# Kernel optimization log

Measured on AMD Instinct MI355X. Metric: run time of the kernel, lower is better.

The kernel has to match this reference:

```python
import jax, jax.numpy as jnp
import numpy as np
from jax import lax

DATA, WIDTH, BATCH, T = 64, 256, 512, 16
MAX_SUBSTEPS = 8
RTOL, ATOL, SAFETY, FMIN, FMAX = 1e-3, 1e-6, 0.9, 0.2, 10.0

# Tsit5 Butcher tableau (Tsitouras 2011), autonomous field so c-nodes unused.
A21 = 0.161
A31, A32 = -0.008480655492356989, 0.335480655492357
A41, A42, A43 = 2.8971530571054935, -6.359448489975075, 4.3622954328695815
A51, A52, A53, A54 = 5.325864828439257, -11.748883564062828, 7.4955393428898365, -0.09249506636175525
A61, A62, A63, A64, A65 = 5.86145544294642, -12.92096931784711, 8.159367898576159, -0.071584973281401, -0.028269050394068383
B1, B2, B3, B4, B5, B6 = 0.09646076681806523, 0.01, 0.4798896504144996, 1.379008574103742, -3.290069515436081, 2.324710524099774
E1, E2, E3, E4, E5, E6, E7 = -0.001780011052226, -0.000816434459657, 0.007880878010262, -0.144711007173263, 0.582357165452555, -0.458082105929187, 0.015151515151515152


def setup_inputs() -> dict:
    key = jax.random.key(0)
    ks = jax.random.split(key, 4)
    ts = jnp.linspace(0.0, 1.0, T, dtype=jnp.float32)
    y0 = jax.random.normal(ks[0], (BATCH, DATA), dtype=jnp.float32)
    s_in = 1.0 / np.sqrt(DATA)
    s_w = 1.0 / np.sqrt(WIDTH)
    W0 = jax.random.normal(ks[1], (WIDTH, DATA), dtype=jnp.float32) * s_in
    b0 = jnp.zeros((WIDTH,), dtype=jnp.float32)
    W1 = jax.random.normal(ks[2], (WIDTH, WIDTH), dtype=jnp.float32) * s_w
    b1 = jnp.zeros((WIDTH,), dtype=jnp.float32)
    W2 = jax.random.normal(ks[3], (DATA, WIDTH), dtype=jnp.float32) * s_w
    b2 = jnp.zeros((DATA,), dtype=jnp.float32)
    return {"ts": ts, "y0": y0, "W0": W0, "b0": b0, "W1": W1, "b1": b1, "W2": W2, "b2": b2}


def _mlp(y, W0, b0, W1, b1, W2, b2):
    h = jax.nn.softplus(W0 @ y + b0)
    h = jax.nn.softplus(W1 @ h + b1)
    return W2 @ h + b2


def _tsit5_step(f, y, dt):
    k1 = f(y)
    k2 = f(y + dt * (A21 * k1))
    k3 = f(y + dt * (A31 * k1 + A32 * k2))
    k4 = f(y + dt * (A41 * k1 + A42 * k2 + A43 * k3))
    k5 = f(y + dt * (A51 * k1 + A52 * k2 + A53 * k3 + A54 * k4))
    k6 = f(y + dt * (A61 * k1 + A62 * k2 + A63 * k3 + A64 * k4 + A65 * k5))
    y_new = y + dt * (B1 * k1 + B2 * k2 + B3 * k3 + B4 * k4 + B5 * k5 + B6 * k6)
    k7 = f(y_new)  # FSAL stage, used only in the embedded error estimate here
    err = dt * (E1 * k1 + E2 * k2 + E3 * k3 + E4 * k4 + E5 * k5 + E6 * k6 + E7 * k7)
    return y_new, err


def _solve(ts, y0, Wb):
    f = lambda y: _mlp(y, *Wb)
    dt0 = ts[1] - ts[0]
    pairs = jnp.stack([ts[:-1], ts[1:]], axis=1)  # [T-1, 2]

    def interval(carry, pair):
        y, dt = carry
        t0, t1 = pair[0], pair[1]

        def substep(c, _):
            t, y, dt = c
            rem = t1 - t
            done = rem <= 1e-6
            dt_c = jnp.where(done, dt, jnp.minimum(dt, rem))
            y_new, err = _tsit5_step(f, y, dt_c)
            scale = ATOL + RTOL * jnp.maximum(jnp.abs(y), jnp.abs(y_new))
            err_norm = jnp.sqrt(jnp.mean((err / scale) ** 2))
            accept = err_norm <= 1.0
            # integral (I) controller, order-5 method -> exponent -1/5
            factor = jnp.clip(SAFETY * jnp.maximum(err_norm, 1e-10) ** (-0.2), FMIN, FMAX)
            step = jnp.logical_and(accept, jnp.logical_not(done))
            t_n = jnp.where(step, t + dt_c, t)
            y_n = jnp.where(step, y_new, y)
            dt_n = jnp.where(done, dt, dt_c * factor)
            return (t_n, y_n, dt_n), None

        (_, yF, dtF), _ = lax.scan(substep, (t0, y, dt), None, length=MAX_SUBSTEPS)
        return (yF, dtF), yF

    _, ys_tail = lax.scan(interval, (y0, dt0), pairs)
    return jnp.concatenate([y0[None], ys_tail], axis=0)  # [T, DATA]


def reference(ts, y0, W0, b0, W1, b1, W2, b2):
    Wb = (W0, b0, W1, b1, W2, b2)
    return jax.vmap(lambda y: _solve(ts, y, Wb))(y0)  # [BATCH, T, DATA]
```

## Files before the change

### kernel.cpp

```cpp
#include <hip/hip_runtime.h>
#include <math.h>

#define DATA 64
#define WIDTH 256
#define BATCHN 512
#define TPTS 16
#define MAXSUB 8
#define NSAMP 2
#define NBLK (BATCHN / NSAMP)
#define NTHR 512

#define RTOLc 1e-3f
#define ATOLc 1e-6f
#define SAFETYc 0.9f
#define FMINc 0.2f
#define FMAXc 10.0f

#define A21 0.161f
#define A31 (-0.008480655492356989f)
#define A32 0.335480655492357f
#define A41 2.8971530571054935f
#define A42 (-6.359448489975075f)
#define A43 4.3622954328695815f
#define A51 5.325864828439257f
#define A52 (-11.748883564062828f)
#define A53 7.4955393428898365f
#define A54 (-0.09249506636175525f)
#define A61 5.86145544294642f
#define A62 (-12.92096931784711f)
#define A63 8.159367898576159f
#define A64 (-0.071584973281401f)
#define A65 (-0.028269050394068383f)
#define B1c 0.09646076681806523f
#define B2c 0.01f
#define B3c 0.4798896504144996f
#define B4c 1.379008574103742f
#define B5c (-3.290069515436081f)
#define B6c 2.324710524099774f
#define E1c (-0.001780011052226f)
#define E2c (-0.000816434459657f)
#define E3c 0.007880878010262f
#define E4c (-0.144711007173263f)
#define E5c 0.582357165452555f
#define E6c (-0.458082105929187f)
#define E7c 0.015151515151515152f

__device__ __forceinline__ float softplus_jax(float x) {
    return fmaxf(x, 0.0f) + log1pf(expf(-fabsf(x)));
}

#define DOT4(acc, wq, xv)                                                     \
    acc = fmaf((wq).x, (xv).x, acc); acc = fmaf((wq).y, (xv).y, acc);         \
    acc = fmaf((wq).z, (xv).z, acc); acc = fmaf((wq).w, (xv).w, acc);

#define FEVAL_CORE(PIN0, PIN1)                                                \
    {         \
        const float4* xx0 = reinterpret_cast<const float4*>((PIN0) + h * 32); \
        const float4* xx1 = reinterpret_cast<const float4*>((PIN1) + h * 32); \
        float a0 = 0.f, a1 = 0.f, c0 = 0.f, c1 = 0.f;                         \
        _Pragma("unroll")                                                     \
        for (int j = 0; j < 8; j += 2) {                                      \
            float4 u = xx0[j], v = xx1[j];                                    \
            DOT4(a0, w0q[j], u); DOT4(a1, w0q[j], v);                         \
            float4 u2 = xx0[j + 1], v2 = xx1[j + 1];                          \
            DOT4(c0, w0q[j + 1], u2); DOT4(c1, w0q[j + 1], v2);               \
        }                                                                     \
        s_ps0[0][h][r] = a0 + c0;                                             \
        s_ps0[1][h][r] = a1 + c1;                                             \
    }                                                                         \
    __syncthreads();                                                          \
                                \
    s_h0[h][r] = softplus_jax(s_ps0[h][0][r] + s_ps0[h][1][r] + s_b0[r]);     \
    __syncthreads();                                                          \
    {                           \
        const float4* xx0 = reinterpret_cast<const float4*>(&s_h0[0][h * 128]); \
        const float4* xx1 = reinterpret_cast<const float4*>(&s_h0[1][h * 128]); \
        float a0 = 0.f, a1 = 0.f, c0 = 0.f, c1 = 0.f;                         \
        _Pragma("unroll")                                                     \
        for (int j = 0; j < 32; j += 2) {                                     \
            float4 u = xx0[j], v = xx1[j];                                    \
            DOT4(a0, w1q[j], u); DOT4(a1, w1q[j], v);                         \
            float4 u2 = xx0[j + 1], v2 = xx1[j + 1];                          \
            DOT4(c0, w1q[j + 1], u2); DOT4(c1, w1q[j + 1], v2);               \
        }                                                                     \
        s_ps1[0][h][r] = a0 + c0;                                             \
        s_ps1[1][h][r] = a1 + c1;                                             \
    }                                                                         \
    __syncthreads();                                                          \
    s_h1[h][r] = softplus_jax(s_ps1[h][0][r] + s_ps1[h][1][r] + s_b1[r]);     \
    __syncthreads();                                                          \
    {    \
        const float4* xx0 = reinterpret_cast<const float4*>(&s_h1[0][kc * 32]); \
        const float4* xx1 = reinterpret_cast<const float4*>(&s_h1[1][kc * 32]); \
        float a0 = 0.f, a1 = 0.f;                                             \
        _Pragma("unroll")                                                     \
        for (int j = 0; j < 8; ++j) {                                         \
            float4 u = xx0[j], v = xx1[j];                                    \
            const int kb = kc * 32 + j * 4;                                   \
            float wa = sW2T[kb + 0][d], wb = sW2T[kb + 1][d];                 \
            float wc = sW2T[kb + 2][d], wd = sW2T[kb + 3][d];                 \
            a0 = fmaf(wa, u.x, a0); a1 = fmaf(wa, v.x, a1);                   \
            a0 = fmaf(wb, u.y, a0); a1 = fmaf(wb, v.y, a1);                   \
            a0 = fmaf(wc, u.z, a0); a1 = fmaf(wc, v.z, a1);                   \
            a0 = fmaf(wd, u.w, a0); a1 = fmaf(wd, v.w, a1);                   \
        }                                                                     \
        s_ps2[0][kc][d] = a0;                                                 \
        s_ps2[1][kc][d] = a1;                                                 \
    }                                                                         \
    __syncthreads();

#define KV_SUM(s)                                                             \
    (((s_ps2[s][0][d] + s_ps2[s][1][d]) + (s_ps2[s][2][d] + s_ps2[s][3][d]))  \
   + ((s_ps2[s][4][d] + s_ps2[s][5][d]) + (s_ps2[s][6][d] + s_ps2[s][7][d]))  \
   + s_b2[d])

__global__ __launch_bounds__(NTHR, 2)
void ode_kernel(const float* __restrict__ ts, const float* __restrict__ y0,
                const float* __restrict__ W0, const float* __restrict__ b0,
                const float* __restrict__ W1, const float* __restrict__ b1,
                const float* __restrict__ W2, const float* __restrict__ b2,
                float* __restrict__ out)
{
    __shared__ __align__(16) float sW2T[WIDTH][DATA];
    __shared__ __align__(16) float s_y[NSAMP][DATA];
    __shared__ __align__(16) float s_yst[NSAMP][DATA];
    __shared__ __align__(16) float s_ynew[NSAMP][DATA];
    __shared__ __align__(16) float s_k[NSAMP][6][DATA];
    __shared__ __align__(16) float s_h0[NSAMP][WIDTH];
    __shared__ __align__(16) float s_h1[NSAMP][WIDTH];
    __shared__ __align__(16) float s_ps0[NSAMP][2][WIDTH];
    __shared__ __align__(16) float s_ps1[NSAMP][2][WIDTH];
    __shared__ __align__(16) float s_ps2[NSAMP][8][DATA];
    __shared__ float s_b0[WIDTH], s_b1[WIDTH], s_b2[DATA];
    __shared__ float s_err[NSAMP];

    const int t  = threadIdx.x;
    const int r  = t & 255;
    const int h  = t >> 8;
    const int d  = t & 63;
    const int kc = t >> 6;
    const int b  = blockIdx.x;

    float4 w0q[8], w1q[32];
    {
        const float4* p0 = reinterpret_cast<const float4*>(W0 + r * DATA + h * 32);
#pragma unroll
        for (int j = 0; j < 8; ++j) w0q[j] = p0[j];
        const float4* p1 = reinterpret_cast<const float4*>(W1 + r * WIDTH + h * 128);
#pragma unroll
        for (int j = 0; j < 32; ++j) w1q[j] = p1[j];
    }
    for (int i = t; i < WIDTH * DATA; i += NTHR) {
        const int k = i >> 6, dd = i & 63;
        sW2T[k][dd] = W2[dd * WIDTH + k];
    }
    if (t < WIDTH) { s_b0[t] = b0[t]; s_b1[t] = b1[t]; }
    if (t < DATA)  { s_b2[t] = b2[t]; }
    if (t < NSAMP * DATA) {
        const int s = t >> 6;
        const float v = y0[(b * NSAMP + s) * DATA + d];
        s_y[s][d] = v;
        out[(size_t)(b * NSAMP + s) * TPTS * DATA + d] = v;
    }
    __syncthreads();

    float dtv0 = ts[1] - ts[0];
    float dtv1 = dtv0;

    for (int iv = 0; iv < TPTS - 1; ++iv) {
        const float t1v = ts[iv + 1];
        float tc0 = ts[iv], tc1 = tc0;

        for (int ss = 0; ss < MAXSUB; ++ss) {
            const float rem0 = t1v - tc0, rem1 = t1v - tc1;
            const bool done0 = rem0 <= 1e-6f, done1 = rem1 <= 1e-6f;
            if (done0 && done1) break;
            const float dtc0 = done0 ? dtv0 : fminf(dtv0, rem0);
            const float dtc1 = done1 ? dtv1 : fminf(dtv1, rem1);

            FEVAL_CORE(&s_y[0][0], &s_y[1][0])
            if (t < 128) {
                const int s = kc;
                const float dtc_s = (s == 0) ? dtc0 : dtc1;
                const float kv = KV_SUM(s);
                s_k[s][0][d] = kv;
                s_yst[s][d] = s_y[s][d] + dtc_s * (A21 * kv);
            }
            __syncthreads();
            FEVAL_CORE(&s_yst[0][0], &s_yst[1][0])
            if (t < 128) {
                const int s = kc;
                const float dtc_s = (s == 0) ? dtc0 : dtc1;
                const float kv = KV_SUM(s);
                s_k[s][1][d] = kv;
                s_yst[s][d] = s_y[s][d] + dtc_s * (A31 * s_k[s][0][d] + A32 * kv);
            }
            __syncthreads();
            FEVAL_CORE(&s_yst[0][0], &s_yst[1][0])
            if (t < 128) {
                const int s = kc;
                const float dtc_s = (s == 0) ? dtc0 : dtc1;
                const float kv = KV_SUM(s);
                s_k[s][2][d] = kv;
                s_yst[s][d] = s_y[s][d] + dtc_s * (A41 * s_k[s][0][d] + A42 * s_k[s][1][d] + A43 * kv);
            }
            __syncthreads();
            FEVAL_CORE(&s_yst[0][0], &s_yst[1][0])
            if (t < 128) {
                const int s = kc;
                const float dtc_s = (s == 0) ? dtc0 : dtc1;
                const float kv = KV_SUM(s);
                s_k[s][3][d] = kv;
                s_yst[s][d] = s_y[s][d] + dtc_s * (A51 * s_k[s][0][d] + A52 * s_k[s][1][d]
                                                 + A53 * s_k[s][2][d] + A54 * kv);
            }
            __syncthreads();
            FEVAL_CORE(&s_yst[0][0], &s_yst[1][0])
            if (t < 128) {
                const int s = kc;
                const float dtc_s = (s == 0) ? dtc0 : dtc1;
                const float kv = KV_SUM(s);
                s_k[s][4][d] = kv;
                s_yst[s][d] = s_y[s][d] + dtc_s * (A61 * s_k[s][0][d] + A62 * s_k[s][1][d]
                                                 + A63 * s_k[s][2][d] + A64 * s_k[s][3][d] + A65 * kv);
            }
            __syncthreads();
            FEVAL_CORE(&s_yst[0][0], &s_yst[1][0])
            if (t < 128) {
                const int s = kc;
                const float dtc_s = (s == 0) ? dtc0 : dtc1;
                const float kv = KV_SUM(s);
                s_k[s][5][d] = kv;
                s_ynew[s][d] = s_y[s][d] + dtc_s * (B1c * s_k[s][0][d] + B2c * s_k[s][1][d]
                                                  + B3c * s_k[s][2][d] + B4c * s_k[s][3][d]
                                                  + B5c * s_k[s][4][d] + B6c * kv);
            }
            __syncthreads();
            FEVAL_CORE(&s_ynew[0][0], &s_ynew[1][0])
            if (t < 128) {
                const int s = kc;
                const float dtc_s = (s == 0) ? dtc0 : dtc1;
                const float kv = KV_SUM(s);
                const float e = dtc_s * (E1c * s_k[s][0][d] + E2c * s_k[s][1][d]
                                       + E3c * s_k[s][2][d] + E4c * s_k[s][3][d]
                                       + E5c * s_k[s][4][d] + E6c * s_k[s][5][d] + E7c * kv);
                const float yv = s_y[s][d], ynv = s_ynew[s][d];
                const float sc = ATOLc + RTOLc * fmaxf(fabsf(yv), fabsf(ynv));
                const float rr = e / sc;
                float v = rr * rr;
#pragma unroll
                for (int off = 32; off > 0; off >>= 1) v += __shfl_xor(v, off, 64);
                if (d == 0) s_err[s] = v;
            }
            __syncthreads();

            const float en0 = sqrtf(s_err[0] * (1.0f / DATA));
            const float en1 = sqrtf(s_err[1] * (1.0f / DATA));
            const bool acc0 = en0 <= 1.0f, acc1 = en1 <= 1.0f;
            float f0 = fminf(fmaxf(SAFETYc * powf(fmaxf(en0, 1e-10f), -0.2f), FMINc), FMAXc);
            float f1 = fminf(fmaxf(SAFETYc * powf(fmaxf(en1, 1e-10f), -0.2f), FMINc), FMAXc);
            const bool step0 = acc0 && !done0, step1 = acc1 && !done1;
            if (t < 128) {
                const int s = kc;
                const bool st = (s == 0) ? step0 : step1;
                if (st) s_y[s][d] = s_ynew[s][d];
            }
            if (step0) tc0 += dtc0;
            if (step1) tc1 += dtc1;
            dtv0 = done0 ? dtv0 : dtc0 * f0;
            dtv1 = done1 ? dtv1 : dtc1 * f1;
            __syncthreads();
        }

        if (t < 128) {
            const int s = kc;
            out[(size_t)(b * NSAMP + s) * TPTS * DATA + (size_t)(iv + 1) * DATA + d] = s_y[s][d];
        }
    }
}

extern "C" void kernel_launch(void* const* d_in, const int* in_sizes, int n_in,
                              void* d_out, int out_size, void* d_ws, size_t ws_size,
                              hipStream_t stream)
{
    const float* ts = (const float*)d_in[0];
    const float* y0 = (const float*)d_in[1];
    const float* W0 = (const float*)d_in[2];
    const float* b0 = (const float*)d_in[3];
    const float* W1 = (const float*)d_in[4];
    const float* b1 = (const float*)d_in[5];
    const float* W2 = (const float*)d_in[6];
    const float* b2 = (const float*)d_in[7];
    float* out = (float*)d_out;

    ode_kernel<<<NBLK, NTHR, 0, stream>>>(ts, y0, W0, b0, W1, b1, W2, b2, out);
}
```

Measured before the change: 444.2 us.

## Double block threads to 1024 and move W0 to transposed shared memory

```diff
diff --git a/kernel.cpp b/kernel.cpp
--- a/kernel.cpp
+++ b/kernel.cpp
@@ -8,7 +8,7 @@
 #define MAXSUB 8
 #define NSAMP 2
 #define NBLK (BATCHN / NSAMP)
-#define NTHR 512
+#define NTHR 1024
 
 #define RTOLc 1e-3f
 #define ATOLc 1e-6f
@@ -54,84 +54,81 @@
     acc = fmaf((wq).z, (xv).z, acc); acc = fmaf((wq).w, (xv).w, acc);
 
 #define FEVAL_CORE(PIN0, PIN1)                                                \
-    {         \
-        const float4* xx0 = reinterpret_cast<const float4*>((PIN0) + h * 32); \
-        const float4* xx1 = reinterpret_cast<const float4*>((PIN1) + h * 32); \
+    {                                                            \
+        const float* x0 = (PIN0) + h * 16;                                    \
+        const float* x1 = (PIN1) + h * 16;                                    \
+        float a0 = 0.f, a1 = 0.f;                                             \
+        _Pragma("unroll")                                                     \
+        for (int kk = 0; kk < 16; ++kk) {                                     \
+            const float w = sW0T[h * 16 + kk][r];                             \
+            a0 = fmaf(w, x0[kk], a0); a1 = fmaf(w, x1[kk], a1);               \
+        }                                                                     \
+        s_ps[0][h][r] = a0; s_ps[1][h][r] = a1;                               \
+    }                                                                         \
+    __syncthreads();                                                          \
+    if (t < 512) {                                                            \
+        const int s = t >> 8;                                                 \
+        s_h0[s][r] = softplus_jax(((s_ps[s][0][r] + s_ps[s][1][r])            \
+                                 + (s_ps[s][2][r] + s_ps[s][3][r])) + b0r);   \
+    }                                                                         \
+    __syncthreads();                                                          \
+    {                                                            \
+        const float4* x0 = reinterpret_cast<const float4*>(&s_h0[0][h * 64]); \
+        const float4* x1 = reinterpret_cast<const float4*>(&s_h0[1][h * 64]); \
         float a0 = 0.f, a1 = 0.f, c0 = 0.f, c1 = 0.f;                         \
         _Pragma("unroll")                                                     \
-        for (int j = 0; j < 8; j += 2) {                                      \
-            float4 u = xx0[j], v = xx1[j];                                    \
-            DOT4(a0, w0q[j], u); DOT4(a1, w0q[j], v);                         \
-            float4 u2 = xx0[j + 1], v2 = xx1[j + 1];                          \
-            DOT4(c0, w0q[j + 1], u2); DOT4(c1, w0q[j + 1], v2);               \
-        }                                                                     \
-        s_ps0[0][h][r] = a0 + c0;                                             \
-        s_ps0[1][h][r] = a1 + c1;                                             \
-    }                                                                         \
-    __syncthreads();                                                          \
-                                \
-    s_h0[h][r] = softplus_jax(s_ps0[h][0][r] + s_ps0[h][1][r] + s_b0[r]);     \
-    __syncthreads();                                                          \
-    {                           \
-        const float4* xx0 = reinterpret_cast<const float4*>(&s_h0[0][h * 128]); \
-        const float4* xx1 = reinterpret_cast<const float4*>(&s_h0[1][h * 128]); \
-        float a0 = 0.f, a1 = 0.f, c0 = 0.f, c1 = 0.f;                         \
-        _Pragma("unroll")                                                     \
-        for (int j = 0; j < 32; j += 2) {                                     \
-            float4 u = xx0[j], v = xx1[j];                                    \
+        for (int j = 0; j < 16; j += 2) {                                     \
+            float4 u = x0[j], v = x1[j];                                      \
             DOT4(a0, w1q[j], u); DOT4(a1, w1q[j], v);                         \
-            float4 u2 = xx0[j + 1], v2 = xx1[j + 1];                          \
+            float4 u2 = x0[j + 1], v2 = x1[j + 1];                            \
             DOT4(c0, w1q[j + 1], u2); DOT4(c1, w1q[j + 1], v2);               \
         }                                                                     \
-        s_ps1[0][h][r] = a0 + c0;                                             \
-        s_ps1[1][h][r] = a1 + c1;                                             \
-    }                                                                         \
-    __syncthreads();                                                          \
-    s_h1[h][r] = softplus_jax(s_ps1[h][0][r] + s_ps1[h][1][r] + s_b1[r]);     \
-    __syncthreads();                                                          \
-    {    \
-        const float4* xx0 = reinterpret_cast<const float4*>(&s_h1[0][kc * 32]); \
-        const float4* xx1 = reinterpret_cast<const float4*>(&s_h1[1][kc * 32]); \
+        s_ps[0][h][r] = a0 + c0; s_ps[1][h][r] = a1 + c1;                     \
+    }                                                                         \
+    __syncthreads();                                                          \
+    if (t < 512) {                                                            \
+        const int s = t >> 8;                                                 \
+        s_h1[s][r] = softplus_jax(((s_ps[s][0][r] + s_ps[s][1][r])            \
+                                 + (s_ps[s][2][r] + s_ps[s][3][r])) + b1r);   \
+    }                                                                         \
+    __syncthreads();                                                          \
+    {                                                            \
+        const float* x0 = &s_h1[0][kc * 16];                                  \
+        const float* x1 = &s_h1[1][kc * 16];                                  \
         float a0 = 0.f, a1 = 0.f;                                             \
         _Pragma("unroll")                                                     \
-        for (int j = 0; j < 8; ++j) {                                         \
-            float4 u = xx0[j], v = xx1[j];                                    \
-            const int kb = kc * 32 + j * 4;                                   \
-            float wa = sW2T[kb + 0][d], wb = sW2T[kb + 1][d];                 \
-            float wc = sW2T[kb + 2][d], wd = sW2T[kb + 3][d];                 \
-            a0 = fmaf(wa, u.x, a0); a1 = fmaf(wa, v.x, a1);                   \
-            a0 = fmaf(wb, u.y, a0); a1 = fmaf(wb, v.y, a1);                   \
-            a0 = fmaf(wc, u.z, a0); a1 = fmaf(wc, v.z, a1);                   \
-            a0 = fmaf(wd, u.w, a0); a1 = fmaf(wd, v.w, a1);                   \
+        for (int kk = 0; kk < 16; ++kk) {                                     \
+            const float w = sW2T[kc * 16 + kk][d];                            \
+            a0 = fmaf(w, x0[kk], a0); a1 = fmaf(w, x1[kk], a1);               \
         }                                                                     \
-        s_ps2[0][kc][d] = a0;                                                 \
-        s_ps2[1][kc][d] = a1;                                                 \
+        s_ps2[0][kc][d] = a0; s_ps2[1][kc][d] = a1;                           \
     }                                                                         \
     __syncthreads();
 
 #define KV_SUM(s)                                                             \
-    (((s_ps2[s][0][d] + s_ps2[s][1][d]) + (s_ps2[s][2][d] + s_ps2[s][3][d]))  \
-   + ((s_ps2[s][4][d] + s_ps2[s][5][d]) + (s_ps2[s][6][d] + s_ps2[s][7][d]))  \
-   + s_b2[d])
-
-__global__ __launch_bounds__(NTHR, 2)
+    (((((s_ps2[s][0][d] + s_ps2[s][1][d]) + (s_ps2[s][2][d] + s_ps2[s][3][d]))  \
+     + ((s_ps2[s][4][d] + s_ps2[s][5][d]) + (s_ps2[s][6][d] + s_ps2[s][7][d]))) \
+    + (((s_ps2[s][8][d] + s_ps2[s][9][d]) + (s_ps2[s][10][d] + s_ps2[s][11][d]))\
+     + ((s_ps2[s][12][d] + s_ps2[s][13][d]) + (s_ps2[s][14][d] + s_ps2[s][15][d])))) \
+    + b2d)
+
+__global__ __launch_bounds__(NTHR)
 void ode_kernel(const float* __restrict__ ts, const float* __restrict__ y0,
                 const float* __restrict__ W0, const float* __restrict__ b0,
                 const float* __restrict__ W1, const float* __restrict__ b1,
                 const float* __restrict__ W2, const float* __restrict__ b2,
                 float* __restrict__ out)
 {
+    __shared__ __align__(16) float sW0T[DATA][WIDTH];
     __shared__ __align__(16) float sW2T[WIDTH][DATA];
+    __shared__ __align__(16) float s_ps[NSAMP][4][WIDTH];
+    __shared__ __align__(16) float s_ps2[NSAMP][16][DATA];
+    __shared__ __align__(16) float s_h0[NSAMP][WIDTH];
+    __shared__ __align__(16) float s_h1[NSAMP][WIDTH];
     __shared__ __align__(16) float s_y[NSAMP][DATA];
     __shared__ __align__(16) float s_yst[NSAMP][DATA];
     __shared__ __align__(16) float s_ynew[NSAMP][DATA];
     __shared__ __align__(16) float s_k[NSAMP][6][DATA];
-    __shared__ __align__(16) float s_h0[NSAMP][WIDTH];
-    __shared__ __align__(16) float s_h1[NSAMP][WIDTH];
-    __shared__ __align__(16) float s_ps0[NSAMP][2][WIDTH];
-    __shared__ __align__(16) float s_ps1[NSAMP][2][WIDTH];
-    __shared__ __align__(16) float s_ps2[NSAMP][8][DATA];
-    __shared__ float s_b0[WIDTH], s_b1[WIDTH], s_b2[DATA];
     __shared__ float s_err[NSAMP];
 
     const int t  = threadIdx.x;
@@ -141,21 +138,23 @@
     const int kc = t >> 6;
     const int b  = blockIdx.x;
 
-    float4 w0q[8], w1q[32];
+    float4 w1q[16];
     {
-        const float4* p0 = reinterpret_cast<const float4*>(W0 + r * DATA + h * 32);
+        const float4* p1 = reinterpret_cast<const float4*>(W1 + r * WIDTH + h * 64);
 #pragma unroll
-        for (int j = 0; j < 8; ++j) w0q[j] = p0[j];
-        const float4* p1 = reinterpret_cast<const float4*>(W1 + r * WIDTH + h * 128);
-#pragma unroll
-        for (int j = 0; j < 32; ++j) w1q[j] = p1[j];
-    }
-    for (int i = t; i < WIDTH * DATA; i += NTHR) {
-        const int k = i >> 6, dd = i & 63;
-        sW2T[k][dd] = W2[dd * WIDTH + k];
-    }
-    if (t < WIDTH) { s_b0[t] = b0[t]; s_b1[t] = b1[t]; }
-    if (t < DATA)  { s_b2[t] = b2[t]; }
+        for (int j = 0; j < 16; ++j) w1q[j] = p1[j];
+    }
+    for (int i = t; i < DATA * WIDTH; i += NTHR) {
+        const int rr = i >> 6, kk = i & 63;
+        sW0T[kk][rr] = W0[i];
+    }
+    for (int i = t; i < DATA * WIDTH; i += NTHR) {
+        const int dd = i >> 8, kk = i & 255;
+        sW2T[kk][dd] = W2[i];
+    }
+    const float b0r = b0[r];
+    const float b1r = b1[r];
+    const float b2d = b2[d];
     if (t < NSAMP * DATA) {
         const int s = t >> 6;
         const float v = y0[(b * NSAMP + s) * DATA + d];
@@ -180,7 +179,7 @@
 
             FEVAL_CORE(&s_y[0][0], &s_y[1][0])
             if (t < 128) {
-                const int s = kc;
+                const int s = t >> 6;
                 const float dtc_s = (s == 0) ? dtc0 : dtc1;
                 const float kv = KV_SUM(s);
                 s_k[s][0][d] = kv;
@@ -189,7 +188,7 @@
             __syncthreads();
             FEVAL_CORE(&s_yst[0][0], &s_yst[1][0])
             if (t < 128) {
-                const int s = kc;
+                const int s = t >> 6;
                 const float dtc_s = (s == 0) ? dtc0 : dtc1;
                 const float kv = KV_SUM(s);
                 s_k[s][1][d] = kv;
@@ -198,7 +197,7 @@
             __syncthreads();
             FEVAL_CORE(&s_yst[0][0], &s_yst[1][0])
             if (t < 128) {
-                const int s = kc;
+                const int s = t >> 6;
                 const float dtc_s = (s == 0) ? dtc0 : dtc1;
                 const float kv = KV_SUM(s);
                 s_k[s][2][d] = kv;
@@ -207,7 +206,7 @@
             __syncthreads();
             FEVAL_CORE(&s_yst[0][0], &s_yst[1][0])
             if (t < 128) {
-                const int s = kc;
+                const int s = t >> 6;
                 const float dtc_s = (s == 0) ? dtc0 : dtc1;
                 const float kv = KV_SUM(s);
                 s_k[s][3][d] = kv;
@@ -217,7 +216,7 @@
             __syncthreads();
             FEVAL_CORE(&s_yst[0][0], &s_yst[1][0])
             if (t < 128) {
-                const int s = kc;
+                const int s = t >> 6;
                 const float dtc_s = (s == 0) ? dtc0 : dtc1;
                 const float kv = KV_SUM(s);
                 s_k[s][4][d] = kv;
@@ -227,7 +226,7 @@
             __syncthreads();
             FEVAL_CORE(&s_yst[0][0], &s_yst[1][0])
             if (t < 128) {
-                const int s = kc;
+                const int s = t >> 6;
                 const float dtc_s = (s == 0) ? dtc0 : dtc1;
                 const float kv = KV_SUM(s);
                 s_k[s][5][d] = kv;
@@ -238,7 +237,7 @@
             __syncthreads();
             FEVAL_CORE(&s_ynew[0][0], &s_ynew[1][0])
             if (t < 128) {
-                const int s = kc;
+                const int s = t >> 6;
                 const float dtc_s = (s == 0) ? dtc0 : dtc1;
                 const float kv = KV_SUM(s);
                 const float e = dtc_s * (E1c * s_k[s][0][d] + E2c * s_k[s][1][d]
@@ -246,8 +245,8 @@
                                        + E5c * s_k[s][4][d] + E6c * s_k[s][5][d] + E7c * kv);
                 const float yv = s_y[s][d], ynv = s_ynew[s][d];
                 const float sc = ATOLc + RTOLc * fmaxf(fabsf(yv), fabsf(ynv));
-                const float rr = e / sc;
-                float v = rr * rr;
+                const float rr2 = e / sc;
+                float v = rr2 * rr2;
 #pragma unroll
                 for (int off = 32; off > 0; off >>= 1) v += __shfl_xor(v, off, 64);
                 if (d == 0) s_err[s] = v;
@@ -261,7 +260,7 @@
             float f1 = fminf(fmaxf(SAFETYc * powf(fmaxf(en1, 1e-10f), -0.2f), FMINc), FMAXc);
             const bool step0 = acc0 && !done0, step1 = acc1 && !done1;
             if (t < 128) {
-                const int s = kc;
+                const int s = t >> 6;
                 const bool st = (s == 0) ? step0 : step1;
                 if (st) s_y[s][d] = s_ynew[s][d];
             }
@@ -273,7 +272,7 @@
         }
 
         if (t < 128) {
-            const int s = kc;
+            const int s = t >> 6;
             out[(size_t)(b * NSAMP + s) * TPTS * DATA + (size_t)(iv + 1) * DATA + d] = s_y[s][d];
         }
     }
```

New measurement: 469.2 us. 1.06x slower.
